# Kernel optimization log

Measured on AMD Instinct MI355X. Metric: run time of the kernel, lower is better.

The kernel has to match this reference:

```python
import jax, jax.numpy as jnp
import numpy as np

NUM_HEADS = 16

def _stablemax3_s(x):
    # 3rd-order Taylor approx of exp(x), Eq 38
    pos = 1.0 + x * (1.0 + 0.5 * x * (1.0 + x / 3.0))
    neg = 1.0 / (1.0 - x * (1.0 - 0.5 * x * (1.0 - x / 3.0)))
    return jnp.where(x >= 0, pos, neg)

def stablemax3(logits, axis=-1):
    logits = logits - jnp.max(logits, axis=axis, keepdims=True)
    s = _stablemax3_s(logits)
    return s / jnp.sum(s, axis=axis, keepdims=True)

def setup_inputs() -> dict:
    key = jax.random.key(0)
    k1, k2, k3 = jax.random.split(key, 3)
    B, S, D = 2, 2048, 1024
    x = jax.random.normal(k1, (B, S, D), dtype=jnp.float32)
    w_qkv = jax.random.normal(k2, (3 * D, D), dtype=jnp.float32) * 0.02
    w_out = jax.random.normal(k3, (D, D), dtype=jnp.float32) * 0.02
    b_out = jnp.zeros((D,), dtype=jnp.float32)
    return {"x": x, "w_qkv": w_qkv, "w_out": w_out, "b_out": b_out}

def reference(x, w_qkv, w_out, b_out):
    B, S, D = x.shape
    H = NUM_HEADS
    hd = D // H
    scale = hd ** (-0.5)
    qkv = x @ w_qkv.T                                  # [B, S, 3D]
    qkv = qkv.reshape(B, S, 3, H, hd)
    qkv = jnp.transpose(qkv, (2, 0, 3, 1, 4))          # [3, B, H, S, hd]
    q, k, v = qkv[0], qkv[1], qkv[2]                   # pos(.) is identity here
    attn = jnp.einsum('bhsd,bhtd->bhst', q, k) * scale # [B, H, S, S]
    attn = stablemax3(attn, axis=-1)
    out = jnp.einsum('bhst,bhtd->bhsd', attn, v)       # [B, H, S, hd]
    out = jnp.transpose(out, (0, 2, 1, 3)).reshape(B, S, D)
    return out @ w_out.T + b_out
```

## Files before the change

kernel.cpp:

```cpp
#include <hip/hip_runtime.h>

typedef _Float16 half8 __attribute__((ext_vector_type(8)));
typedef _Float16 half4 __attribute__((ext_vector_type(4)));
typedef _Float16 half2v __attribute__((ext_vector_type(2)));
typedef float floatx4 __attribute__((ext_vector_type(4)));
typedef unsigned int uint2v __attribute__((ext_vector_type(2)));
typedef unsigned int uint4v __attribute__((ext_vector_type(4)));

__device__ __forceinline__ void gl_lds16(const _Float16* g, _Float16* l) {
    __builtin_amdgcn_global_load_lds(
        (const __attribute__((address_space(1))) void*)g,
        (__attribute__((address_space(3))) void*)l, 16, 0, 0);
}

__device__ __forceinline__ half2v cvt_pk(float a, float b) {
    return __builtin_bit_cast(half2v, __builtin_amdgcn_cvt_pkrtz(a, b));
}

__device__ __forceinline__ half2v rcp2(half2v d) {
#if __has_builtin(__builtin_amdgcn_rcph)
    half2v r;
    r[0] = __builtin_amdgcn_rcph(d[0]);
    r[1] = __builtin_amdgcn_rcph(d[1]);
    return r;
#else
    half2v r;
    r[0] = (_Float16)__builtin_amdgcn_rcpf((float)d[0]);
    r[1] = (_Float16)__builtin_amdgcn_rcpf((float)d[1]);
    return r;
#endif
}

__device__ __forceinline__ float dot2acc(half2v a, float acc) {
#if __has_builtin(__builtin_amdgcn_fdot2)
    const half2v one = {(_Float16)1.0f, (_Float16)1.0f};
    return __builtin_amdgcn_fdot2(a, one, acc, false);
#else
    return acc + (float)a[0] + (float)a[1];
#endif
}

__device__ __forceinline__ half8 from4(half2v a, half2v b, half2v c, half2v d) {
    uint4v u = {__builtin_bit_cast(unsigned int, a), __builtin_bit_cast(unsigned int, b),
                __builtin_bit_cast(unsigned int, c), __builtin_bit_cast(unsigned int, d)};
    return __builtin_bit_cast(half8, u);
}

__device__ __forceinline__ half8 from_lohi(half4 lo, half4 hi) {
    uint2v l = __builtin_bit_cast(uint2v, lo);
    uint2v h = __builtin_bit_cast(uint2v, hi);
    uint4v u = {l[0], l[1], h[0], h[1]};
    return __builtin_bit_cast(half8, u);
}

__global__ __launch_bounds__(256) void cvt_xw(const floatx4* __restrict__ x,
                                              const floatx4* __restrict__ wq,
                                              half4* __restrict__ xh,
                                              half4* __restrict__ wqh) {
    int i = blockIdx.x * 256 + threadIdx.x;
    floatx4 v;
    half4 h;
    if (i < 1048576) {
        v = x[i];
#pragma unroll
        for (int j = 0; j < 4; ++j) h[j] = (_Float16)v[j];
        xh[i] = h;
    } else {
        int j4 = i - 1048576;
        v = wq[j4];
#pragma unroll
        for (int j = 0; j < 4; ++j) h[j] = (_Float16)v[j];
        wqh[j4] = h;
    }
}

__global__ __launch_bounds__(256) void cvt_f32_f16(const floatx4* __restrict__ in,
                                                   half4* __restrict__ out, int n4) {
    int i = blockIdx.x * 256 + threadIdx.x;
    if (i >= n4) return;
    floatx4 v = in[i];
    half4 h;
#pragma unroll
    for (int j = 0; j < 4; ++j) h[j] = (_Float16)v[j];
    out[i] = h;
}

__global__ __launch_bounds__(256) void gemm_qkv(const _Float16* __restrict__ A,
                                                const _Float16* __restrict__ B,
                                                _Float16* __restrict__ qh,
                                                _Float16* __restrict__ kh,
                                                _Float16* __restrict__ vth) {
    const int K = 1024;
    __shared__ _Float16 SH[128 * 68];
    _Float16* As = SH;
    _Float16* Bs = SH + 4096;
    const int t = threadIdx.x;
    const int lane = t & 63, w = t >> 6;
    const int l15 = lane & 15, quad = lane >> 4;
    const int wm = w >> 1, wn = w & 1;
    const int m0 = blockIdx.y * 128, n0 = blockIdx.x * 128;

    floatx4 acc[4][4];
    const floatx4 zf = {0.f, 0.f, 0.f, 0.f};
#pragma unroll
    for (int i = 0; i < 4; ++i)
#pragma unroll
        for (int j = 0; j < 4; ++j) acc[i][j] = zf;

    for (int kt = 0; kt < K; kt += 32) {
        __syncthreads();
#pragma unroll
        for (int it = 0; it < 2; ++it) {
            int cc = it * 256 + t;
            int row = cc >> 2, kc = cc & 3;
            gl_lds16(&A[(size_t)(m0 + row) * K + kt + kc * 8], &As[cc * 8]);
            gl_lds16(&B[(size_t)(n0 + row) * K + kt + kc * 8], &Bs[cc * 8]);
        }
        __syncthreads();
        half8 af[4], bfr[4];
#pragma unroll
        for (int i = 0; i < 4; ++i)
            af[i] = *(const half8*)&As[(wm * 64 + i * 16 + l15) * 32 + quad * 8];
#pragma unroll
        for (int i = 0; i < 4; ++i)
            bfr[i] = *(const half8*)&Bs[(wn * 64 + i * 16 + l15) * 32 + quad * 8];
#pragma unroll
        for (int mi = 0; mi < 4; ++mi)
#pragma unroll
            for (int ni = 0; ni < 4; ++ni)
                acc[mi][ni] = __builtin_amdgcn_mfma_f32_16x16x32_f16(af[mi], bfr[ni],
                                                                     acc[mi][ni], 0, 0, 0);
    }

    const int b = m0 >> 11, s0 = m0 & 2047;
#pragma unroll
    for (int hf = 0; hf < 2; ++hf) {
        __syncthreads();
        if (wn == hf) {
#pragma unroll
            for (int mi = 0; mi < 4; ++mi)
#pragma unroll
                for (int ni = 0; ni < 4; ++ni)
#pragma unroll
                    for (int r = 0; r < 4; ++r)
                        SH[(wm * 64 + mi * 16 + quad * 4 + r) * 68 + ni * 16 + l15] =
                            (_Float16)acc[mi][ni][r];
        }
        __syncthreads();
        const int cbase = n0 + hf * 64;
        if (n0 < 2048) {
            const int hh = (cbase & 1023) >> 6;
            _Float16* dst = (n0 < 1024 ? qh : kh) + (size_t)((b << 4) | hh) * 131072;
#pragma unroll
            for (int it = 0; it < 4; ++it) {
                int cc = it * 256 + t;
                int r = cc >> 3, c8 = cc & 7;
                half4 lo = *(const half4*)&SH[r * 68 + c8 * 8];
                half4 hi = *(const half4*)&SH[r * 68 + c8 * 8 + 4];
                *(half8*)&dst[(size_t)(s0 + r) * 64 + c8 * 8] = from_lohi(lo, hi);
            }
        } else {
            const int hh = (cbase - 2048) >> 6;
            _Float16* dst = vth + (size_t)((b << 4) | hh) * 131072;
#pragma unroll
            for (int it = 0; it < 4; ++it) {
                int cc = it * 256 + t;
                int d = cc >> 4, s8 = cc & 15;
                int sq = s8 & 7;
                int base = (s8 >> 3) * 64 + (sq >> 2) * 32 + (sq & 3) * 4;
                half8 v;
#pragma unroll
                for (int j = 0; j < 8; ++j)
                    v[j] = SH[(base + (j >> 2) * 16 + (j & 3)) * 68 + d];
                *(half8*)&dst[(size_t)d * 2048 + s0 + s8 * 8] = v;
            }
        }
    }
}

__global__ __launch_bounds__(256) void gemm_out(const _Float16* __restrict__ A,
                                                const _Float16* __restrict__ B,
                                                float* __restrict__ C,
                                                const float* __restrict__ bias) {
    const int K = 1024, N = 1024;
    __shared__ _Float16 SH[6144];
    _Float16* As = SH;
    _Float16* Bs = SH + 2048;
    const int t = threadIdx.x;
    const int lane = t & 63, w = t >> 6;
    const int l15 = lane & 15, quad = lane >> 4;
    const int wm = w >> 1, wn = w & 1;
    const int m0 = blockIdx.y * 64, n0 = blockIdx.x * 128;

    floatx4 acc[2][4];
    const floatx4 zf = {0.f, 0.f, 0.f, 0.f};
#pragma unroll
    for (int i = 0; i < 2; ++i)
#pragma unroll
        for (int j = 0; j < 4; ++j) acc[i][j] = zf;

    for (int kt = 0; kt < K; kt += 32) {
        __syncthreads();
        {
            int row = t >> 2, kc = t & 3;
            gl_lds16(&A[(size_t)(m0 + row) * K + kt + kc * 8], &As[t * 8]);
        }
#pragma unroll
        for (int it = 0; it < 2; ++it) {
            int cc = it * 256 + t;
            int row = cc >> 2, kc = cc & 3;
            gl_lds16(&B[(size_t)(n0 + row) * K + kt + kc * 8], &Bs[cc * 8]);
        }
        __syncthreads();
        half8 af[2], bfr[4];
#pragma unroll
        for (int i = 0; i < 2; ++i)
            af[i] = *(const half8*)&As[(wm * 32 + i * 16 + l15) * 32 + quad * 8];
#pragma unroll
        for (int i = 0; i < 4; ++i)
            bfr[i] = *(const half8*)&Bs[(wn * 64 + i * 16 + l15) * 32 + quad * 8];
#pragma unroll
        for (int mi = 0; mi < 2; ++mi)
#pragma unroll
            for (int ni = 0; ni < 4; ++ni)
                acc[mi][ni] = __builtin_amdgcn_mfma_f32_16x16x32_f16(af[mi], bfr[ni],
                                                                     acc[mi][ni], 0, 0, 0);
    }

#pragma unroll
    for (int mi = 0; mi < 2; ++mi) {
#pragma unroll
        for (int ni = 0; ni < 4; ++ni) {
            int col = n0 + wn * 64 + ni * 16 + l15;
            float bv = bias[col];
#pragma unroll
            for (int r = 0; r < 4; ++r) {
                int row = m0 + wm * 32 + mi * 16 + quad * 4 + r;
                C[(size_t)row * N + col] = acc[mi][ni][r] + bv;
            }
        }
    }
}

__global__ __launch_bounds__(256, 4) void attn_kernel(const _Float16* __restrict__ qh,
                                                      const _Float16* __restrict__ kh,
                                                      const _Float16* __restrict__ vth,
                                                      _Float16* __restrict__ out) {
    __shared__ _Float16 SM[16384];

    const int t = threadIdx.x;
    const int lane = t & 63, w = t >> 6;
    const int l15 = lane & 15, quad = lane >> 4;
    const int sw = l15 & 7;
    const int qg = w >> 1, kg = w & 1;
    const int bh = blockIdx.x;
    const int q0 = blockIdx.y * 64;
    const int b = bh >> 4, h = bh & 15;

    const _Float16* Qp = qh + (size_t)bh * 131072 + q0 * 64;
    const _Float16* Kp = kh + (size_t)bh * 131072;
    const _Float16* VTp = vth + (size_t)bh * 131072;

    const int row0 = t >> 3, cg0 = (t & 7) ^ (row0 & 7);
    const _Float16* K0 = &Kp[(size_t)row0 * 64 + cg0 * 8];
    const _Float16* K1 = &Kp[(size_t)(32 + row0) * 64 + cg0 * 8];
    const _Float16* V0 = &VTp[(size_t)row0 * 2048 + cg0 * 8];
    const _Float16* V1 = &VTp[(size_t)(32 + row0) * 2048 + cg0 * 8];

    const floatx4 zf = {0.f, 0.f, 0.f, 0.f};

    half8 qf[2][2];
#pragma unroll
    for (int nh = 0; nh < 2; ++nh)
#pragma unroll
        for (int kk = 0; kk < 2; ++kk) {
            half8 q = *(const half8*)&Qp[(qg * 32 + nh * 16 + l15) * 64 + kk * 32 + quad * 8];
#pragma unroll
            for (int j = 0; j < 8; ++j) q[j] = q[j] * (_Float16)0.125f;
            qf[nh][kk] = q;
        }

    float rmax[2] = {-1.0e30f, -1.0e30f};
    gl_lds16(K0, &SM[t * 8]);
    gl_lds16(K1, &SM[2048 + t * 8]);
    __syncthreads();
    for (int kt = 0, cur = 0; kt < 2048; kt += 64, cur ^= 1) {
        if (kt + 64 < 2048) {
            _Float16* kd = cur ? &SM[0] : &SM[4096];
            gl_lds16(K0 + (size_t)(kt + 64) * 64, kd + t * 8);
            gl_lds16(K1 + (size_t)(kt + 64) * 64, kd + 2048 + t * 8);
        }
        const _Float16* Ks = cur ? &SM[4096] : &SM[0];
        floatx4 sa[2][2];
#pragma unroll
        for (int Ti = 0; Ti < 2; ++Ti) { sa[Ti][0] = zf; sa[Ti][1] = zf; }
#pragma unroll
        for (int kk = 0; kk < 2; ++kk) {
            half8 kf[2];
#pragma unroll
            for (int Ti = 0; Ti < 2; ++Ti)
                kf[Ti] = *(const half8*)&Ks[(((kg * 2 + Ti) * 16 + l15) << 6) +
                                            ((((kk << 2) + quad) ^ sw) << 3)];
            __builtin_amdgcn_s_setprio(1);
#pragma unroll
            for (int Ti = 0; Ti < 2; ++Ti)
#pragma unroll
                for (int nh = 0; nh < 2; ++nh)
                    sa[Ti][nh] = __builtin_amdgcn_mfma_f32_16x16x32_f16(kf[Ti], qf[nh][kk],
                                                                        sa[Ti][nh], 0, 0, 0);
            __builtin_amdgcn_s_setprio(0);
        }
#pragma unroll
        for (int Ti = 0; Ti < 2; ++Ti)
#pragma unroll
            for (int nh = 0; nh < 2; ++nh)
#pragma unroll
                for (int r = 0; r < 4; ++r)
                    rmax[nh] = fmaxf(rmax[nh], sa[Ti][nh][r]);
        __syncthreads();
    }
#pragma unroll
    for (int nh = 0; nh < 2; ++nh) {
        rmax[nh] = fmaxf(rmax[nh], __shfl_xor(rmax[nh], 16, 64));
        rmax[nh] = fmaxf(rmax[nh], __shfl_xor(rmax[nh], 32, 64));
    }
    {
        float* EXM = (float*)SM;
        if (quad == 0) {
#pragma unroll
            for (int nh = 0; nh < 2; ++nh)
                EXM[((qg * 2 + nh) * 2 + kg) * 16 + l15] = rmax[nh];
        }
        __syncthreads();
#pragma unroll
        for (int nh = 0; nh < 2; ++nh)
            rmax[nh] = fmaxf(EXM[((qg * 2 + nh) * 2 + 0) * 16 + l15],
                             EXM[((qg * 2 + nh) * 2 + 1) * 16 + l15]);
        __syncthreads();
    }
    const floatx4 xmv[2] = {{-rmax[0], -rmax[0], -rmax[0], -rmax[0]},
                            {-rmax[1], -rmax[1], -rmax[1], -rmax[1]}};

    const half2v cA = {(_Float16)(-1.0f / 6.0f), (_Float16)(-1.0f / 6.0f)};
    const half2v cB = {(_Float16)0.5f, (_Float16)0.5f};
    const half2v cC = {(_Float16)-1.0f, (_Float16)-1.0f};
    const half2v cD = {(_Float16)1.0f, (_Float16)1.0f};

    float rsum[2] = {0.f, 0.f};
    floatx4 oacc[4][2];
#pragma unroll
    for (int i = 0; i < 4; ++i) { oacc[i][0] = zf; oacc[i][1] = zf; }

    gl_lds16(K0, &SM[t * 8]);
    gl_lds16(K1, &SM[2048 + t * 8]);
    gl_lds16(V0, &SM[8192 + t * 8]);
    gl_lds16(V1, &SM[8192 + 2048 + t * 8]);
    __syncthreads();
    for (int kt = 0, cur = 0; kt < 2048; kt += 64, cur ^= 1) {
        if (kt + 64 < 2048) {
            _Float16* kd = cur ? &SM[0] : &SM[4096];
            _Float16* vd = cur ? &SM[8192] : &SM[12288];
            gl_lds16(K0 + (size_t)(kt + 64) * 64, kd + t * 8);
            gl_lds16(K1 + (size_t)(kt + 64) * 64, kd + 2048 + t * 8);
            gl_lds16(V0 + (kt + 64), vd + t * 8);
            gl_lds16(V1 + (kt + 64), vd + 2048 + t * 8);
        }
        const _Float16* Ks = cur ? &SM[4096] : &SM[0];
        const _Float16* VTs = cur ? &SM[12288] : &SM[8192];

        floatx4 sa[2][2];
#pragma unroll
        for (int Ti = 0; Ti < 2; ++Ti) { sa[Ti][0] = xmv[0]; sa[Ti][1] = xmv[1]; }
#pragma unroll
        for (int kk = 0; kk < 2; ++kk) {
            half8 kf[2];
#pragma unroll
            for (int Ti = 0; Ti < 2; ++Ti)
                kf[Ti] = *(const half8*)&Ks[(((kg * 2 + Ti) * 16 + l15) << 6) +
                                            ((((kk << 2) + quad) ^ sw) << 3)];
            __builtin_amdgcn_s_setprio(1);
#pragma unroll
            for (int Ti = 0; Ti < 2; ++Ti)
#pragma unroll
                for (int nh = 0; nh < 2; ++nh)
                    sa[Ti][nh] = __builtin_amdgcn_mfma_f32_16x16x32_f16(kf[Ti], qf[nh][kk],
                                                                        sa[Ti][nh], 0, 0, 0);
            __builtin_amdgcn_s_setprio(0);
        }
        half8 vf[4];
#pragma unroll
        for (int di = 0; di < 4; ++di)
            vf[di] = *(const half8*)&VTs[((di * 16 + l15) << 6) +
                                         ((((kg << 2) + quad) ^ sw) << 3)];
#pragma unroll
        for (int nh = 0; nh < 2; ++nh) {
            half2v p2m[4];
#pragma unroll
            for (int m = 0; m < 4; ++m) {
                int Ti = m >> 1;
                int r0 = (m & 1) * 2;
                half2v x2 = cvt_pk(sa[Ti][nh][r0], sa[Ti][nh][r0 + 1]);
                half2v hp = __builtin_elementwise_fma(x2, cA, cB);
                hp = __builtin_elementwise_fma(x2, hp, cC);
                hp = __builtin_elementwise_fma(x2, hp, cD);
                half2v p2 = rcp2(hp);
                rsum[nh] = dot2acc(p2, rsum[nh]);
                p2m[m] = p2;
            }
            half8 pb = from4(p2m[0], p2m[1], p2m[2], p2m[3]);
            __builtin_amdgcn_s_setprio(1);
#pragma unroll
            for (int di = 0; di < 4; ++di)
                oacc[di][nh] = __builtin_amdgcn_mfma_f32_16x16x32_f16(vf[di], pb,
                                                                      oacc[di][nh], 0, 0, 0);
            __builtin_amdgcn_s_setprio(0);
        }
        __syncthreads();
    }

#pragma unroll
    for (int nh = 0; nh < 2; ++nh) {
        rsum[nh] += __shfl_xor(rsum[nh], 16, 64);
        rsum[nh] += __shfl_xor(rsum[nh], 32, 64);
    }

    float* EXO = (float*)SM;
    float* EXS = (float*)(SM + 8192);
    _Float16* Os = SM + 8320;
    if (kg) {
#pragma unroll
        for (int nh = 0; nh < 2; ++nh)
#pragma unroll
            for (int di = 0; di < 4; ++di)
                *(floatx4*)&EXO[(((((qg * 2 + nh) * 4 + di) * 4 + quad) * 16) + l15) * 4] =
                    oacc[di][nh];
        if (quad == 0) {
#pragma unroll
            for (int nh = 0; nh < 2; ++nh)
                EXS[(qg * 2 + nh) * 16 + l15] = rsum[nh];
        }
    }
    __syncthreads();
    if (!kg) {
        float inv[2];
#pragma unroll
        for (int nh = 0; nh < 2; ++nh)
            inv[nh] = 1.0f / (rsum[nh] + EXS[(qg * 2 + nh) * 16 + l15]);
#pragma unroll
        for (int nh = 0; nh < 2; ++nh)
#pragma unroll
            for (int di = 0; di < 4; ++di) {
                floatx4 part = *(const floatx4*)
                    &EXO[(((((qg * 2 + nh) * 4 + di) * 4 + quad) * 16) + l15) * 4];
                half4 hv;
#pragma unroll
                for (int r = 0; r < 4; ++r)
                    hv[r] = (_Float16)((oacc[di][nh][r] + part[r]) * inv[nh]);
                *(half4*)&Os[(qg * 32 + nh * 16 + l15) * 72 + di * 16 + quad * 4] = hv;
            }
    }
    __syncthreads();
    _Float16* Op = out + (size_t)(b * 2048 + q0) * 1024 + h * 64;
#pragma unroll
    for (int it = 0; it < 2; ++it) {
        int cc = it * 256 + t;
        int r = cc >> 3, c8 = cc & 7;
        *(half8*)&Op[(size_t)r * 1024 + c8 * 8] = *(const half8*)&Os[r * 72 + c8 * 8];
    }
}

extern "C" void kernel_launch(void* const* d_in, const int* in_sizes, int n_in,
                              void* d_out, int out_size, void* d_ws, size_t ws_size,
                              hipStream_t stream) {
    const float* x_f = (const float*)d_in[0];
    const float* wqkv_f = (const float*)d_in[1];
    const float* wout_f = (const float*)d_in[2];
    const float* bias_f = (const float*)d_in[3];

    char* ws = (char*)d_ws;
    _Float16* xh = (_Float16*)(ws);
    _Float16* aoh = xh;
    _Float16* wqh = (_Float16*)(ws + 8388608);
    _Float16* woh = wqh;
    _Float16* qh = (_Float16*)(ws + 14680064);
    _Float16* kh = (_Float16*)(ws + 23068672);
    _Float16* vth = (_Float16*)(ws + 31457280);

    cvt_xw<<<7168, 256, 0, stream>>>((const floatx4*)x_f, (const floatx4*)wqkv_f,
                                     (half4*)xh, (half4*)wqh);
    gemm_qkv<<<dim3(24, 32), 256, 0, stream>>>(xh, wqh, qh, kh, vth);
    cvt_f32_f16<<<1024, 256, 0, stream>>>((const floatx4*)wout_f, (half4*)woh, 262144);
    attn_kernel<<<dim3(32, 32), 256, 0, stream>>>(qh, kh, vth, aoh);
    gemm_out<<<dim3(8, 64), 256, 0, stream>>>(aoh, woh, (float*)d_out, bias_f);
}
```

Before: 207.6 us.

## Enlarge max-pass K tile to 128 rows and unroll PV loop by two

The first pass, which computes the row maximum, now processes 128-key tiles per iteration using the full 16K-half LDS as a double buffer. That halves its barrier count and raises MFMA work per sync. The second pass is manually unrolled by two through a lambda with fixed buffer addresses, which removes the cur-select pointer arithmetic. It also starts the MFMA accumulators from zero or the negated max directly, so no separate init is needed. Register pressure rises in the first pass (8 accumulators, 8 K fragments), which may hurt occupancy.

New measurement: 204.1 us. About the same (-1.7%).

```diff
diff --git a/kernel.cpp b/kernel.cpp
--- a/kernel.cpp
+++ b/kernel.cpp
@@ -263,9 +263,7 @@
 
     const int row0 = t >> 3, cg0 = (t & 7) ^ (row0 & 7);
     const _Float16* K0 = &Kp[(size_t)row0 * 64 + cg0 * 8];
-    const _Float16* K1 = &Kp[(size_t)(32 + row0) * 64 + cg0 * 8];
     const _Float16* V0 = &VTp[(size_t)row0 * 2048 + cg0 * 8];
-    const _Float16* V1 = &VTp[(size_t)(32 + row0) * 2048 + cg0 * 8];
 
     const floatx4 zf = {0.f, 0.f, 0.f, 0.f};
 
@@ -281,43 +279,52 @@
         }
 
     float rmax[2] = {-1.0e30f, -1.0e30f};
-    gl_lds16(K0, &SM[t * 8]);
-    gl_lds16(K1, &SM[2048 + t * 8]);
+#pragma unroll
+    for (int s = 0; s < 4; ++s)
+        gl_lds16(K0 + s * 2048, &SM[s * 2048 + t * 8]);
     __syncthreads();
-    for (int kt = 0, cur = 0; kt < 2048; kt += 64, cur ^= 1) {
-        if (kt + 64 < 2048) {
-            _Float16* kd = cur ? &SM[0] : &SM[4096];
-            gl_lds16(K0 + (size_t)(kt + 64) * 64, kd + t * 8);
-            gl_lds16(K1 + (size_t)(kt + 64) * 64, kd + 2048 + t * 8);
-        }
-        const _Float16* Ks = cur ? &SM[4096] : &SM[0];
-        floatx4 sa[2][2];
-#pragma unroll
-        for (int Ti = 0; Ti < 2; ++Ti) { sa[Ti][0] = zf; sa[Ti][1] = zf; }
-#pragma unroll
-        for (int kk = 0; kk < 2; ++kk) {
-            half8 kf[2];
-#pragma unroll
-            for (int Ti = 0; Ti < 2; ++Ti)
-                kf[Ti] = *(const half8*)&Ks[(((kg * 2 + Ti) * 16 + l15) << 6) +
-                                            ((((kk << 2) + quad) ^ sw) << 3)];
+    {
+        const _Float16* sKp = K0 + 8192;
+        for (int i = 0, cur = 0; i < 16; ++i, cur ^= 1) {
+            if (i < 15) {
+                _Float16* kd = cur ? &SM[0] : &SM[8192];
+#pragma unroll
+                for (int s = 0; s < 4; ++s)
+                    gl_lds16(sKp + s * 2048, kd + s * 2048 + t * 8);
+                sKp += 8192;
+            }
+            const _Float16* Ks = cur ? &SM[8192] : &SM[0];
+            half8 kf0[4], kf1[4];
+#pragma unroll
+            for (int Ti = 0; Ti < 4; ++Ti) {
+                const int rb = ((kg * 4 + Ti) * 16 + l15) << 6;
+                kf0[Ti] = *(const half8*)&Ks[rb + ((quad ^ sw) << 3)];
+                kf1[Ti] = *(const half8*)&Ks[rb + (((4 + quad) ^ sw) << 3)];
+            }
+            floatx4 sa[4][2];
             __builtin_amdgcn_s_setprio(1);
 #pragma unroll
-            for (int Ti = 0; Ti < 2; ++Ti)
+            for (int Ti = 0; Ti < 4; ++Ti)
 #pragma unroll
                 for (int nh = 0; nh < 2; ++nh)
-                    sa[Ti][nh] = __builtin_amdgcn_mfma_f32_16x16x32_f16(kf[Ti], qf[nh][kk],
+                    sa[Ti][nh] = __builtin_amdgcn_mfma_f32_16x16x32_f16(kf0[Ti], qf[nh][0],
+                                                                        zf, 0, 0, 0);
+#pragma unroll
+            for (int Ti = 0; Ti < 4; ++Ti)
+#pragma unroll
+                for (int nh = 0; nh < 2; ++nh)
+                    sa[Ti][nh] = __builtin_amdgcn_mfma_f32_16x16x32_f16(kf1[Ti], qf[nh][1],
                                                                         sa[Ti][nh], 0, 0, 0);
             __builtin_amdgcn_s_setprio(0);
-        }
-#pragma unroll
-        for (int Ti = 0; Ti < 2; ++Ti)
-#pragma unroll
-            for (int nh = 0; nh < 2; ++nh)
-#pragma unroll
-                for (int r = 0; r < 4; ++r)
-                    rmax[nh] = fmaxf(rmax[nh], sa[Ti][nh][r]);
-        __syncthreads();
+#pragma unroll
+            for (int Ti = 0; Ti < 4; ++Ti)
+#pragma unroll
+                for (int nh = 0; nh < 2; ++nh)
+#pragma unroll
+                    for (int r = 0; r < 4; ++r)
+                        rmax[nh] = fmaxf(rmax[nh], sa[Ti][nh][r]);
+            __syncthreads();
+        }
     }
 #pragma unroll
     for (int nh = 0; nh < 2; ++nh) {
@@ -351,42 +358,29 @@
 #pragma unroll
     for (int i = 0; i < 4; ++i) { oacc[i][0] = zf; oacc[i][1] = zf; }
 
-    gl_lds16(K0, &SM[t * 8]);
-    gl_lds16(K1, &SM[2048 + t * 8]);
-    gl_lds16(V0, &SM[8192 + t * 8]);
-    gl_lds16(V1, &SM[8192 + 2048 + t * 8]);
-    __syncthreads();
-    for (int kt = 0, cur = 0; kt < 2048; kt += 64, cur ^= 1) {
-        if (kt + 64 < 2048) {
-            _Float16* kd = cur ? &SM[0] : &SM[4096];
-            _Float16* vd = cur ? &SM[8192] : &SM[12288];
-            gl_lds16(K0 + (size_t)(kt + 64) * 64, kd + t * 8);
-            gl_lds16(K1 + (size_t)(kt + 64) * 64, kd + 2048 + t * 8);
-            gl_lds16(V0 + (kt + 64), vd + t * 8);
-            gl_lds16(V1 + (kt + 64), vd + 2048 + t * 8);
-        }
-        const _Float16* Ks = cur ? &SM[4096] : &SM[0];
-        const _Float16* VTs = cur ? &SM[12288] : &SM[8192];
-
+    auto tile_step = [&](const _Float16* Ks, const _Float16* VTs) {
+        half8 kf0[2], kf1[2];
+#pragma unroll
+        for (int Ti = 0; Ti < 2; ++Ti) {
+            const int rb = ((kg * 2 + Ti) * 16 + l15) << 6;
+            kf0[Ti] = *(const half8*)&Ks[rb + ((quad ^ sw) << 3)];
+            kf1[Ti] = *(const half8*)&Ks[rb + (((4 + quad) ^ sw) << 3)];
+        }
         floatx4 sa[2][2];
-#pragma unroll
-        for (int Ti = 0; Ti < 2; ++Ti) { sa[Ti][0] = xmv[0]; sa[Ti][1] = xmv[1]; }
-#pragma unroll
-        for (int kk = 0; kk < 2; ++kk) {
-            half8 kf[2];
-#pragma unroll
-            for (int Ti = 0; Ti < 2; ++Ti)
-                kf[Ti] = *(const half8*)&Ks[(((kg * 2 + Ti) * 16 + l15) << 6) +
-                                            ((((kk << 2) + quad) ^ sw) << 3)];
-            __builtin_amdgcn_s_setprio(1);
-#pragma unroll
-            for (int Ti = 0; Ti < 2; ++Ti)
-#pragma unroll
-                for (int nh = 0; nh < 2; ++nh)
-                    sa[Ti][nh] = __builtin_amdgcn_mfma_f32_16x16x32_f16(kf[Ti], qf[nh][kk],
-                                                                        sa[Ti][nh], 0, 0, 0);
-            __builtin_amdgcn_s_setprio(0);
-        }
+        __builtin_amdgcn_s_setprio(1);
+#pragma unroll
+        for (int Ti = 0; Ti < 2; ++Ti)
+#pragma unroll
+            for (int nh = 0; nh < 2; ++nh)
+                sa[Ti][nh] = __builtin_amdgcn_mfma_f32_16x16x32_f16(kf0[Ti], qf[nh][0],
+                                                                    xmv[nh], 0, 0, 0);
+#pragma unroll
+        for (int Ti = 0; Ti < 2; ++Ti)
+#pragma unroll
+            for (int nh = 0; nh < 2; ++nh)
+                sa[Ti][nh] = __builtin_amdgcn_mfma_f32_16x16x32_f16(kf1[Ti], qf[nh][1],
+                                                                    sa[Ti][nh], 0, 0, 0);
+        __builtin_amdgcn_s_setprio(0);
         half8 vf[4];
 #pragma unroll
         for (int di = 0; di < 4; ++di)
@@ -415,7 +409,35 @@
                                                                       oacc[di][nh], 0, 0, 0);
             __builtin_amdgcn_s_setprio(0);
         }
-        __syncthreads();
+    };
+
+    gl_lds16(K0, &SM[t * 8]);
+    gl_lds16(K0 + 2048, &SM[2048 + t * 8]);
+    gl_lds16(V0, &SM[8192 + t * 8]);
+    gl_lds16(V0 + 65536, &SM[8192 + 2048 + t * 8]);
+    __syncthreads();
+
+    {
+        const _Float16* sK = K0 + 4096;
+        const _Float16* sV = V0 + 64;
+        for (int i = 0; i < 16; ++i) {
+            gl_lds16(sK, &SM[4096 + t * 8]);
+            gl_lds16(sK + 2048, &SM[4096 + 2048 + t * 8]);
+            gl_lds16(sV, &SM[12288 + t * 8]);
+            gl_lds16(sV + 65536, &SM[12288 + 2048 + t * 8]);
+            sK += 4096; sV += 64;
+            tile_step(&SM[0], &SM[8192]);
+            __syncthreads();
+            if (i < 15) {
+                gl_lds16(sK, &SM[t * 8]);
+                gl_lds16(sK + 2048, &SM[2048 + t * 8]);
+                gl_lds16(sV, &SM[8192 + t * 8]);
+                gl_lds16(sV + 65536, &SM[8192 + 2048 + t * 8]);
+                sK += 4096; sV += 64;
+            }
+            tile_step(&SM[4096], &SM[12288]);
+            __syncthreads();
+        }
     }
 
 #pragma unroll
```
